# Kernel tuning notes

Hardware: AMD Instinct MI355X
Metric: run time of the kernel (lower is better)

## Reference

```python
import jax, jax.numpy as jnp
import numpy as np
from jax import lax

T, B, H, L = 256, 128, 1024, 4


def setup_inputs() -> dict:
    key = jax.random.key(0)
    ks = jax.random.split(key, 6)
    k = 1.0 / np.sqrt(H)
    inputs = jax.random.normal(ks[0], (T, B, H), dtype=jnp.float32)
    hxs = jax.random.normal(ks[1], (L, B, H), dtype=jnp.float32)
    W_ih = jax.random.uniform(ks[2], (L, H, H), dtype=jnp.float32, minval=-k, maxval=k)
    b_ih = jax.random.uniform(ks[3], (L, H), dtype=jnp.float32, minval=-k, maxval=k)
    W_hh = jax.random.uniform(ks[4], (L, H, H), dtype=jnp.float32, minval=-k, maxval=k)
    b_hh = jax.random.uniform(ks[5], (L, H), dtype=jnp.float32, minval=-k, maxval=k)
    return {"inputs": inputs, "hxs": hxs, "W_ih": W_ih, "b_ih": b_ih, "W_hh": W_hh, "b_hh": b_hh}


def reference(inputs, hxs, W_ih, b_ih, W_hh, b_hh):
    # Multi-layer vanilla tanh RNN, time-major inputs [T, B, H].
    x = inputs
    hns = []
    for i in range(L):
        Wi, bi, Wh, bh = W_ih[i], b_ih[i], W_hh[i], b_hh[i]

        def step(h, x_t):
            h_new = jnp.tanh(x_t @ Wi.T + bi + h @ Wh.T + bh)
            return h_new, h_new

        h_last, outs = lax.scan(step, hxs[i], x)
        x = outs
        hns.append(h_last)
    return x, jnp.stack(hns)
```

## Files before the change

kernel.cpp:

```cpp
#include <hip/hip_runtime.h>


#define TT 256
#define BB 128
#define HH 1024
#define LL 4
#define RING 8
#define MAT (BB * HH)

typedef __attribute__((ext_vector_type(4))) float  float4v;
typedef __attribute__((ext_vector_type(8))) __bf16 bf16x8;
typedef __attribute__((ext_vector_type(8))) unsigned short ushort8;

__device__ inline unsigned short bf16r(float f) {
    union { float f; unsigned u; } v; v.f = f;
    unsigned u = v.u;
    u += 0x7fffu + ((u >> 16) & 1u);
    return (unsigned short)(u >> 16);
}

__device__ inline bf16x8 pack8(float4v a, float4v b) {
    ushort8 r;
    r[0] = bf16r(a[0]); r[1] = bf16r(a[1]); r[2] = bf16r(a[2]); r[3] = bf16r(a[3]);
    r[4] = bf16r(b[0]); r[5] = bf16r(b[1]); r[6] = bf16r(b[2]); r[7] = bf16r(b[3]);
    return __builtin_bit_cast(bf16x8, r);
}

__device__ inline float4v mfma16(bf16x8 a, bf16x8 b, float4v c) {
    return __builtin_amdgcn_mfma_f32_16x16x32_bf16(a, b, c, 0, 0, 0);
}

__device__ inline float fast_tanh(float x) {
    float ax = fabsf(x);
    float e  = __expf(-2.0f * ax);
    float r  = (1.0f - e) / (1.0f + e);
    return copysignf(r, x);
}

__global__ void rnn_prep(const float* __restrict__ hxs,
                         unsigned* __restrict__ F,
                         unsigned short* __restrict__ ring) {
    int i = blockIdx.x * blockDim.x + threadIdx.x;
    if (i < 256) F[i] = 0u;
    int stride = gridDim.x * blockDim.x;
    for (int idx = i; idx < LL * MAT; idx += stride) {
        int g = idx >> 17;
        int rem = idx & (MAT - 1);
        ring[(size_t)(g * RING + RING - 1) * MAT + rem] = bf16r(hxs[idx]);
    }
}

__global__ __launch_bounds__(512, 2) void rnn_pipeline(
    const float* __restrict__ xin,
    const float* __restrict__ Wih,
    const float* __restrict__ bih,
    const float* __restrict__ Whh,
    const float* __restrict__ bhh,
    float* __restrict__ out,
    unsigned* __restrict__ F,
    unsigned short* __restrict__ ring)
{
    const int tid  = threadIdx.x;
    const int lane = tid & 63;
    const int wid  = tid >> 6;
    const int ks   = wid & 3;
    const int mh   = wid >> 2;
    const int g    = blockIdx.x >> 5;
    const int nt   = blockIdx.x & 31;
    const int n0   = nt * 32;

    __shared__ float4v lds_part[8 * 4 * 2 * 64];

    const int rA = lane & 15;
    const int qA = lane >> 4;

    bf16x8 wfrag[2][16];
    {
        const float* Wsrc = (ks < 2) ? (Wih + (size_t)g * HH * HH)
                                     : (Whh + (size_t)g * HH * HH);
        const int kofs = (ks & 1) * 512;
        #pragma unroll
        for (int nt2 = 0; nt2 < 2; ++nt2) {
            const int n = n0 + nt2 * 16 + rA;
            const float* rowp = Wsrc + (size_t)n * HH + kofs + qA * 8;
            #pragma unroll
            for (int ki = 0; ki < 16; ++ki) {
                float4v f0 = *(const float4v*)(rowp + ki * 32);
                float4v f1 = *(const float4v*)(rowp + ki * 32 + 4);
                wfrag[nt2][ki] = pack8(f0, f1);
            }
        }
    }

    const int rest0 = tid >> 6;
    const int nt2r  = rest0 & 1;
    const int mtr   = (rest0 >> 1) & 3;
    const int l2    = lane;
    const int n4    = l2 & 3;
    const int mi    = l2 >> 2;
    const int lidx  = n4 * 16 + mi;
    const int nbase = n0 + nt2r * 16 + n4 * 4;
    float4v biasv;
    {
        float4v bi = *(const float4v*)(bih + (size_t)g * HH + nbase);
        float4v bh = *(const float4v*)(bhh + (size_t)g * HH + nbase);
        biasv = bi + bh;
    }

    const int aoff = (mh * 64 + rA) * HH + (ks & 1) * 512 + qA * 8;
    const bool is_x = (ks < 2);

    const unsigned short* ringL = ring + (size_t)g * RING * MAT;
    const unsigned short* ringP = (g > 0) ? ring + (size_t)(g - 1) * RING * MAT
                                          : (const unsigned short*)0;
    unsigned short* ringM = ring + (size_t)g * RING * MAT;

    for (int t = 0; t < TT; ++t) {
        if (wid == 0) {
            int fidx = g; unsigned tgt = 0u; bool act = false;
            if (lane == 0) {
                act = true; tgt = 32u * (unsigned)t;
            } else if (lane == 1 && g > 0) {
                act = true; fidx = g - 1; tgt = 32u * (unsigned)(t + 1);
            } else if (lane == 2 && g < 3 && t >= RING) {
                act = true; fidx = g + 1; tgt = 32u * (unsigned)(t - RING + 1);
            }
            for (;;) {
                bool ok = true;
                if (act) {
                    unsigned v = __hip_atomic_load(F + fidx * 64,
                                     __ATOMIC_RELAXED, __HIP_MEMORY_SCOPE_AGENT);
                    ok = (v >= tgt);
                }
                if (__ballot(!ok) == 0ull) break;
                __builtin_amdgcn_s_sleep(2);
            }
            __builtin_amdgcn_fence(__ATOMIC_ACQUIRE, "agent");
        }
        __syncthreads();

        float4v acc[4][2];
        #pragma unroll
        for (int mt = 0; mt < 4; ++mt) {
            acc[mt][0] = (float4v)0.0f;
            acc[mt][1] = (float4v)0.0f;
        }

        if (is_x && g == 0) {
            const float* xsrc = xin + (size_t)t * MAT;
            #pragma unroll
            for (int ki = 0; ki < 16; ++ki) {
                #pragma unroll
                for (int mt = 0; mt < 4; ++mt) {
                    const float* p = xsrc + aoff + mt * (16 * HH) + ki * 32;
                    float4v f0 = *(const float4v*)p;
                    float4v f1 = *(const float4v*)(p + 4);
                    bf16x8 a = pack8(f0, f1);
                    acc[mt][0] = mfma16(wfrag[0][ki], a, acc[mt][0]);
                    acc[mt][1] = mfma16(wfrag[1][ki], a, acc[mt][1]);
                }
            }
        } else {
            const unsigned short* asrc =
                is_x ? (ringP + (size_t)(t & (RING - 1)) * MAT)
                     : (ringL + (size_t)((t + RING - 1) & (RING - 1)) * MAT);
            const unsigned short* ap = asrc + aoff;
            #pragma unroll
            for (int ki = 0; ki < 16; ++ki) {
                #pragma unroll
                for (int mt = 0; mt < 4; ++mt) {
                    bf16x8 a = *(const bf16x8*)(ap + mt * (16 * HH) + ki * 32);
                    acc[mt][0] = mfma16(wfrag[0][ki], a, acc[mt][0]);
                    acc[mt][1] = mfma16(wfrag[1][ki], a, acc[mt][1]);
                }
            }
        }

        #pragma unroll
        for (int mt = 0; mt < 4; ++mt)
            #pragma unroll
            for (int nt2 = 0; nt2 < 2; ++nt2)
                lds_part[((wid * 4 + mt) * 2 + nt2) * 64 + lane] = acc[mt][nt2];
        __syncthreads();

        unsigned short* ringW = ringM + (size_t)(t & (RING - 1)) * MAT;
        #pragma unroll
        for (int s = 0; s < 2; ++s) {
            float4v sum = lds_part[(((s * 4 + 0) * 4 + mtr) * 2 + nt2r) * 64 + lidx];
            #pragma unroll
            for (int k2 = 1; k2 < 4; ++k2)
                sum += lds_part[(((s * 4 + k2) * 4 + mtr) * 2 + nt2r) * 64 + lidx];
            sum += biasv;
            float vals[4];
            #pragma unroll
            for (int r = 0; r < 4; ++r) vals[r] = fast_tanh(sum[r]);

            const int m = s * 64 + mtr * 16 + mi;
            const size_t eo = (size_t)m * HH + nbase;

            union { unsigned short us[4]; unsigned long long u; } pk;
            #pragma unroll
            for (int r = 0; r < 4; ++r) pk.us[r] = bf16r(vals[r]);
            __hip_atomic_store((unsigned long long*)(ringW + eo), pk.u,
                               __ATOMIC_RELAXED, __HIP_MEMORY_SCOPE_AGENT);

            if (g == 3) {
                float4v o;
                #pragma unroll
                for (int r = 0; r < 4; ++r) o[r] = vals[r];
                *(float4v*)(out + (size_t)t * MAT + eo) = o;
            }
            if (t == TT - 1) {
                float4v o;
                #pragma unroll
                for (int r = 0; r < 4; ++r) o[r] = vals[r];
                *(float4v*)(out + (size_t)TT * MAT + (size_t)g * MAT + eo) = o;
            }
        }

        asm volatile("s_waitcnt vmcnt(0)" ::: "memory");
        __syncthreads();
        if (tid == 0)
            __hip_atomic_fetch_add(F + g * 64, 1u,
                                   __ATOMIC_RELAXED, __HIP_MEMORY_SCOPE_AGENT);
    }
}

extern "C" void kernel_launch(void* const* d_in, const int* in_sizes, int n_in,
                              void* d_out, int out_size, void* d_ws, size_t ws_size,
                              hipStream_t stream) {
    const float* xin = (const float*)d_in[0];
    const float* hxs = (const float*)d_in[1];
    const float* Wih = (const float*)d_in[2];
    const float* bih = (const float*)d_in[3];
    const float* Whh = (const float*)d_in[4];
    const float* bhh = (const float*)d_in[5];
    float* out = (float*)d_out;

    unsigned* F = (unsigned*)d_ws;
    unsigned short* ring = (unsigned short*)((char*)d_ws + 1024);

    rnn_prep<<<256, 256, 0, stream>>>(hxs, F, ring);
    rnn_pipeline<<<128, 512, 0, stream>>>(xin, Wih, bih, Whh, bhh, out, F, ring);
}
```

Before: 8.774 ms.

## Size activation ring to workspace and elide per-step acquire fences

The ring depth is now picked at launch as the largest power of two (up to T) that fits in the workspace, instead of a fixed 8 slots. A deeper ring loosens the back-pressure wait on the next layer and lets the per-step agent-scope acquire fence be skipped: it runs only on ring wraparound, or never when the ring holds all T steps. The spin sleep is also shortened. The risk is coherence: dropping the acquire fence relies on reads of never-reused slots not hitting stale cache lines, which may not be guaranteed by the memory model.

```diff
diff --git a/kernel.cpp b/kernel.cpp
--- a/kernel.cpp
+++ b/kernel.cpp
@@ -5,7 +5,6 @@
 #define BB 128
 #define HH 1024
 #define LL 4
-#define RING 8
 #define MAT (BB * HH)
 
 typedef __attribute__((ext_vector_type(4))) float  float4v;
@@ -39,14 +38,15 @@
 
 __global__ void rnn_prep(const float* __restrict__ hxs,
                          unsigned* __restrict__ F,
-                         unsigned short* __restrict__ ring) {
+                         unsigned short* __restrict__ ring,
+                         int slots) {
     int i = blockIdx.x * blockDim.x + threadIdx.x;
     if (i < 256) F[i] = 0u;
     int stride = gridDim.x * blockDim.x;
     for (int idx = i; idx < LL * MAT; idx += stride) {
         int g = idx >> 17;
         int rem = idx & (MAT - 1);
-        ring[(size_t)(g * RING + RING - 1) * MAT + rem] = bf16r(hxs[idx]);
+        ring[((size_t)g * slots + (slots - 1)) * MAT + rem] = bf16r(hxs[idx]);
     }
 }
 
@@ -58,7 +58,8 @@
     const float* __restrict__ bhh,
     float* __restrict__ out,
     unsigned* __restrict__ F,
-    unsigned short* __restrict__ ring)
+    unsigned short* __restrict__ ring,
+    int slots)
 {
     const int tid  = threadIdx.x;
     const int lane = tid & 63;
@@ -68,6 +69,8 @@
     const int g    = blockIdx.x >> 5;
     const int nt   = blockIdx.x & 31;
     const int n0   = nt * 32;
+    const int smask = slots - 1;
+    const bool may_fence = (slots < TT);
 
     __shared__ float4v lds_part[8 * 4 * 2 * 64];
 
@@ -110,10 +113,10 @@
     const int aoff = (mh * 64 + rA) * HH + (ks & 1) * 512 + qA * 8;
     const bool is_x = (ks < 2);
 
-    const unsigned short* ringL = ring + (size_t)g * RING * MAT;
-    const unsigned short* ringP = (g > 0) ? ring + (size_t)(g - 1) * RING * MAT
+    const unsigned short* ringL = ring + (size_t)g * slots * MAT;
+    const unsigned short* ringP = (g > 0) ? ring + (size_t)(g - 1) * slots * MAT
                                           : (const unsigned short*)0;
-    unsigned short* ringM = ring + (size_t)g * RING * MAT;
+    unsigned short* ringM = ring + (size_t)g * slots * MAT;
 
     for (int t = 0; t < TT; ++t) {
         if (wid == 0) {
@@ -122,8 +125,8 @@
                 act = true; tgt = 32u * (unsigned)t;
             } else if (lane == 1 && g > 0) {
                 act = true; fidx = g - 1; tgt = 32u * (unsigned)(t + 1);
-            } else if (lane == 2 && g < 3 && t >= RING) {
-                act = true; fidx = g + 1; tgt = 32u * (unsigned)(t - RING + 1);
+            } else if (lane == 2 && g < 3 && t >= slots) {
+                act = true; fidx = g + 1; tgt = 32u * (unsigned)(t - slots + 1);
             }
             for (;;) {
                 bool ok = true;
@@ -133,9 +136,10 @@
                     ok = (v >= tgt);
                 }
                 if (__ballot(!ok) == 0ull) break;
-                __builtin_amdgcn_s_sleep(2);
-            }
-            __builtin_amdgcn_fence(__ATOMIC_ACQUIRE, "agent");
+                __builtin_amdgcn_s_sleep(1);
+            }
+            if (may_fence && (t & smask) == 0)
+                __builtin_amdgcn_fence(__ATOMIC_ACQUIRE, "agent");
         }
         __syncthreads();
 
@@ -162,8 +166,8 @@
             }
         } else {
             const unsigned short* asrc =
-                is_x ? (ringP + (size_t)(t & (RING - 1)) * MAT)
-                     : (ringL + (size_t)((t + RING - 1) & (RING - 1)) * MAT);
+                is_x ? (ringP + (size_t)(t & smask) * MAT)
+                     : (ringL + (size_t)((t + slots - 1) & smask) * MAT);
             const unsigned short* ap = asrc + aoff;
             #pragma unroll
             for (int ki = 0; ki < 16; ++ki) {
@@ -183,7 +187,7 @@
                 lds_part[((wid * 4 + mt) * 2 + nt2) * 64 + lane] = acc[mt][nt2];
         __syncthreads();
 
-        unsigned short* ringW = ringM + (size_t)(t & (RING - 1)) * MAT;
+        unsigned short* ringW = ringM + (size_t)(t & smask) * MAT;
         #pragma unroll
         for (int s = 0; s < 2; ++s) {
             float4v sum = lds_part[(((s * 4 + 0) * 4 + mtr) * 2 + nt2r) * 64 + lidx];
@@ -238,8 +242,14 @@
     float* out = (float*)d_out;
 
     unsigned* F = (unsigned*)d_ws;
-    unsigned short* ring = (unsigned short*)((char*)d_ws + 1024);
-
-    rnn_prep<<<256, 256, 0, stream>>>(hxs, F, ring);
-    rnn_pipeline<<<128, 512, 0, stream>>>(xin, Wih, bih, Whh, bhh, out, F, ring);
-}
+    unsigned short* ring = (unsigned short*)((char*)d_ws + 4096);
+
+    int slots = 8;
+    while (slots < TT) {
+        size_t need = 4096 + (size_t)LL * (size_t)(slots * 2) * (size_t)MAT * 2ull;
+        if (need <= ws_size) slots *= 2; else break;
+    }
+
+    rnn_prep<<<256, 256, 0, stream>>>(hxs, F, ring, slots);
+    rnn_pipeline<<<128, 512, 0, stream>>>(xin, Wih, bih, Whh, bhh, out, F, ring, slots);
+}
```

Result: slower. 9.119 ms (+3.9%).
